# Kernel tuning notes

Measured on AMD Instinct MI355X. Metric: run time of the kernel, lower is better.

The kernel has to match this reference:

```python
import jax, jax.numpy as jnp
import numpy as np

N = 100000      # nodes
E = 1600000     # edges (avg degree 16)
F_IN = 512      # input node features
H = 8           # heads in conv1
D = 8           # per-head dim in conv1
C = 7           # classes
NEG_SLOPE = 0.2 # PyG GATConv default leaky_relu slope


def setup_inputs() -> dict:
    key = jax.random.key(0)
    ks = jax.random.split(key, 10)
    s = 0.05
    return {
        "x": jax.random.normal(ks[0], (N, F_IN), jnp.float32),
        "edge_index": jax.random.randint(ks[1], (2, E), 0, N, dtype=jnp.int64),
        "W1": jax.random.normal(ks[2], (F_IN, H * D), jnp.float32) * s,
        "a1_src": jax.random.normal(ks[3], (H, D), jnp.float32) * s,
        "a1_dst": jax.random.normal(ks[4], (H, D), jnp.float32) * s,
        "b1": jnp.zeros((H * D,), jnp.float32),
        "W2": jax.random.normal(ks[5], (H * D, C), jnp.float32) * s,
        "a2_src": jax.random.normal(ks[6], (1, C), jnp.float32) * s,
        "a2_dst": jax.random.normal(ks[7], (1, C), jnp.float32) * s,
        "b2": jnp.zeros((C,), jnp.float32),
    }


def _gat_conv(x, src, dst, W, a_src, a_dst, b, heads, dim, concat, n):
    # linear transform -> [N, H, D]
    h = (x @ W).reshape(n, heads, dim)
    # per-node attention halves: [N, H]
    al_src = jnp.einsum('nhd,hd->nh', h, a_src)
    al_dst = jnp.einsum('nhd,hd->nh', h, a_dst)
    # per-edge logits, leaky relu: [E', H]
    e = jax.nn.leaky_relu(al_src[src] + al_dst[dst], NEG_SLOPE)
    # segment softmax over incoming edges of each dst node
    m = jax.lax.stop_gradient(jax.ops.segment_max(e, dst, num_segments=n))
    p = jnp.exp(e - m[dst])
    z = jax.ops.segment_sum(p, dst, num_segments=n)
    alpha = p / z[dst]                                   # [E', H]
    # weighted scatter-add of source messages -> [N, H, D]
    out = jax.ops.segment_sum(h[src] * alpha[..., None], dst, num_segments=n)
    out = out.reshape(n, heads * dim) if concat else out.mean(axis=1)
    return out + b


def reference(x, edge_index, W1, a1_src, a1_dst, b1, W2, a2_src, a2_dst, b2):
    n = x.shape[0]
    # PyG GATConv default: add self loops
    loops = jnp.arange(n, dtype=edge_index.dtype)
    src = jnp.concatenate([edge_index[0], loops])
    dst = jnp.concatenate([edge_index[1], loops])
    h = _gat_conv(x, src, dst, W1, a1_src, a1_dst, b1, H, D, True, n)
    h = jax.nn.elu(h)
    out = _gat_conv(h, src, dst, W2, a2_src, a2_dst, b2, 1, C, False, n)
    return jax.nn.log_softmax(out, axis=1)
```

## Files before the change

### kernel.cpp

```cpp
#include <hip/hip_runtime.h>
#include <math.h>

#define N_NODES 100000
#define N_EDGES 1600000
#define F_IN 512
#define HD 64
#define CC 7
#define NKT (F_IN / 32)
#define BS 64
#define NBK ((N_NODES + BS - 1) / BS)
#define ECAP 2048
#define SCHUNK 4096
#define SBLK ((N_EDGES + SCHUNK - 1) / SCHUNK)

typedef __attribute__((ext_vector_type(8))) short short8;
typedef __attribute__((ext_vector_type(4))) float f32x4;

__device__ inline unsigned short f2bf(float f) {
    union { float f; unsigned u; } v; v.f = f;
    unsigned u = v.u;
    return (unsigned short)((u + 0x7fffu + ((u >> 16) & 1u)) >> 16);
}
__device__ inline float bf2f(unsigned short b) {
    union { unsigned u; float f; } v; v.u = ((unsigned)b) << 16;
    return v.f;
}

__global__ void zerob_kernel(int* __restrict__ bcur) {
    int i = blockIdx.x * 1024 + threadIdx.x;
    if (i < NBK) bcur[i] = 0;
}

__global__ void w1prep_kernel(const float* __restrict__ W1,
                              unsigned short* __restrict__ wf) {
    int t = blockIdx.x * 256 + threadIdx.x;
    if (t >= NKT * 4 * 64) return;
    int lane = t & 63;
    int ct = (t >> 6) & 3;
    int kt = t >> 8;
    int k0 = kt * 32 + (lane >> 4) * 8;
    int col = ct * 16 + (lane & 15);
    unsigned short* dst = wf + (size_t)t * 8;
    #pragma unroll
    for (int j = 0; j < 8; ++j) dst[j] = f2bf(W1[(k0 + j) * HD + col]);
}

__global__ __launch_bounds__(256) void gemm1att_kernel(const float* __restrict__ x,
                                                       const unsigned short* __restrict__ wf,
                                                       const float* __restrict__ a1s,
                                                       const float* __restrict__ a1d,
                                                       unsigned short* __restrict__ h1b,
                                                       float* __restrict__ als,
                                                       float* __restrict__ ald) {
    __shared__ float ls[64][65];
    const int wave = threadIdx.x >> 6;
    const int lane = threadIdx.x & 63;
    int arow = blockIdx.x * 64 + wave * 16 + (lane & 15);
    if (arow >= N_NODES) arow = N_NODES - 1;
    const float* xp = x + (size_t)arow * F_IN + (lane >> 4) * 8;
    const short8* wp = (const short8*)wf;

    f32x4 acc[4] = {};
    #pragma unroll 4
    for (int kt = 0; kt < NKT; ++kt) {
        f32x4 a0 = *(const f32x4*)(xp + kt * 32);
        f32x4 a1 = *(const f32x4*)(xp + kt * 32 + 4);
        union { short8 s; unsigned short u[8]; } af;
        af.u[0] = f2bf(a0.x); af.u[1] = f2bf(a0.y);
        af.u[2] = f2bf(a0.z); af.u[3] = f2bf(a0.w);
        af.u[4] = f2bf(a1.x); af.u[5] = f2bf(a1.y);
        af.u[6] = f2bf(a1.z); af.u[7] = f2bf(a1.w);
        #pragma unroll
        for (int ct = 0; ct < 4; ++ct) {
            short8 bf = wp[kt * 256 + ct * 64 + lane];
            acc[ct] = __builtin_amdgcn_mfma_f32_16x16x32_bf16(af.s, bf, acc[ct], 0, 0, 0);
        }
    }
    const int lrow_base = wave * 16 + (lane >> 4) * 4;
    const int ocol = lane & 15;
    #pragma unroll
    for (int ct = 0; ct < 4; ++ct) {
        #pragma unroll
        for (int r = 0; r < 4; ++r) {
            int lrow = lrow_base + r;
            int orow = blockIdx.x * 64 + lrow;
            ls[lrow][ct * 16 + ocol] = acc[ct][r];
            if (orow < N_NODES)
                h1b[(size_t)orow * HD + ct * 16 + ocol] = f2bf(acc[ct][r]);
        }
    }
    __syncthreads();
    #pragma unroll
    for (int task = threadIdx.x; task < 64 * 8; task += 256) {
        int r = task >> 3, h = task & 7;
        int node = blockIdx.x * 64 + r;
        if (node < N_NODES) {
            float s = 0.f, d = 0.f;
            #pragma unroll
            for (int k = 0; k < 8; ++k) {
                float v = ls[r][h * 8 + k];
                s += v * a1s[h * 8 + k];
                d += v * a1d[h * 8 + k];
            }
            als[node * 8 + h] = s;
            ald[node * 8 + h] = d;
        }
    }
}

__global__ __launch_bounds__(256) void binscatter_kernel(const int* __restrict__ ei,
                                                         int* __restrict__ bcur,
                                                         int2* __restrict__ pairs) {
    __shared__ int cnt[NBK];
    __shared__ int bas[NBK];
    const int e0 = blockIdx.x * SCHUNK;
    int e1 = e0 + SCHUNK; if (e1 > N_EDGES) e1 = N_EDGES;
    for (int b = threadIdx.x; b < NBK; b += 256) cnt[b] = 0;
    __syncthreads();
    for (int i = e0 + threadIdx.x; i < e1; i += 256)
        atomicAdd(&cnt[ei[N_EDGES + i] >> 6], 1);
    __syncthreads();
    for (int b = threadIdx.x; b < NBK; b += 256) {
        int c = cnt[b];
        bas[b] = c ? atomicAdd(&bcur[b], c) : 0;
        cnt[b] = 0;
    }
    __syncthreads();
    for (int i = e0 + threadIdx.x; i < e1; i += 256) {
        int s = ei[i];
        int t = ei[N_EDGES + i];
        int b = t >> 6;
        int pos = bas[b] + atomicAdd(&cnt[b], 1);
        if (pos < ECAP) pairs[(size_t)b * ECAP + pos] = make_int2(s, t);
    }
}

__global__ __launch_bounds__(256) void gather1_kernel(
        const int* __restrict__ bcur, const int2* __restrict__ pairs,
        const float* __restrict__ als, const float* __restrict__ ald,
        const unsigned short* __restrict__ h1b, const float* __restrict__ b1,
        const float* __restrict__ W2, const float* __restrict__ a2s,
        const float* __restrict__ a2d,
        unsigned short* __restrict__ g2b, float* __restrict__ al2s,
        float* __restrict__ al2d) {
    __shared__ int cnt[BS];
    __shared__ int start[BS];
    __shared__ int srcl[ECAP];
    const int tid = threadIdx.x;
    const int wave = tid >> 6, lane = tid & 63, h = lane >> 3;
    const int e8 = lane & 7, base8 = lane & 56;
    const int n0 = blockIdx.x * BS;
    const int2* bp = pairs + (size_t)blockIdx.x * ECAP;
    int ne = bcur[blockIdx.x]; if (ne > ECAP) ne = ECAP;
    if (tid < BS) cnt[tid] = 0;
    __syncthreads();
    for (int k = tid; k < ne; k += 256)
        atomicAdd(&cnt[bp[k].y & (BS - 1)], 1);
    __syncthreads();
    if (tid < 64) {
        int a = cnt[lane];
        int xx = a;
        #pragma unroll
        for (int o = 1; o < 64; o <<= 1) { int u = __shfl_up(xx, o, 64); if (lane >= o) xx += u; }
        start[lane] = xx - a;
        cnt[lane] = 0;
    }
    __syncthreads();
    for (int k = tid; k < ne; k += 256) {
        int2 pr = bp[k];
        int ln = pr.y & (BS - 1);
        int pos = start[ln] + atomicAdd(&cnt[ln], 1);
        srcl[pos] = pr.x;
    }
    __syncthreads();

    float w[CC];
    #pragma unroll
    for (int c = 0; c < CC; ++c) w[c] = W2[lane * CC + c];
    for (int n = wave * 16; n < wave * 16 + 16; ++n) {
        int node = n0 + n;
        if (node >= N_NODES) break;
        const float aldt = ald[node * 8 + h];
        float e = als[node * 8 + h] + aldt;
        e = (e >= 0.f) ? e : 0.2f * e;
        float p = __expf(e);
        float acc = p * bf2f(h1b[(size_t)node * HD + lane]);
        float z = p;
        int k = start[n];
        const int ke = k + cnt[n];
        for (; k + 8 <= ke; k += 8) {
            int s_own = srcl[k + e8];
            float ee = als[s_own * 8 + h] + aldt;
            ee = (ee >= 0.f) ? ee : 0.2f * ee;
            float pv = __expf(ee);
            #pragma unroll
            for (int q = 0; q < 8; ++q) {
                int se = srcl[k + q];
                float pe = __shfl(pv, base8 | q, 64);
                float ve = bf2f(h1b[(size_t)se * HD + lane]);
                z += pe;
                acc = fmaf(pe, ve, acc);
            }
        }
        if (k < ke) {
            const int m = ke - k;
            int idx = k + ((e8 < m) ? e8 : (m - 1));
            int s_own = srcl[idx];
            float ee = als[s_own * 8 + h] + aldt;
            ee = (ee >= 0.f) ? ee : 0.2f * ee;
            float pv = __expf(ee);
            for (int q = 0; q < m; ++q) {
                int se = srcl[k + q];
                float pe = __shfl(pv, base8 | q, 64);
                float ve = bf2f(h1b[(size_t)se * HD + lane]);
                z += pe;
                acc = fmaf(pe, ve, acc);
            }
        }
        float v = acc / z + b1[lane];
        v = (v > 0.f) ? v : (__expf(v) - 1.f);
        float g[CC];
        #pragma unroll
        for (int c = 0; c < CC; ++c) {
            float r = v * w[c];
            #pragma unroll
            for (int d = 1; d < 64; d <<= 1) r += __shfl_xor(r, d, 64);
            g[c] = r;
        }
        float s2 = 0.f, d2 = 0.f;
        #pragma unroll
        for (int c = 0; c < CC; ++c) { s2 += g[c] * a2s[c]; d2 += g[c] * a2d[c]; }
        if (lane < CC) g2b[(size_t)node * 8 + lane] = f2bf(g[lane]);
        if (lane == CC) g2b[(size_t)node * 8 + CC] = 0;
        if (lane == 8) al2s[node] = s2;
        if (lane == 9) al2d[node] = d2;
    }
}

__global__ __launch_bounds__(256) void gather2_kernel(
        const int* __restrict__ bcur, const int2* __restrict__ pairs,
        const float* __restrict__ al2s, const float* __restrict__ al2d,
        const unsigned short* __restrict__ g2b, const float* __restrict__ b2,
        float* __restrict__ out) {
    __shared__ int cnt[BS];
    __shared__ int start[BS];
    __shared__ int srcl[ECAP];
    const int tid = threadIdx.x;
    const int lane = tid & 63;
    const int grp = tid >> 3, c = tid & 7;
    const int base8 = lane & 56;
    const int n0 = blockIdx.x * BS;
    const int2* bp = pairs + (size_t)blockIdx.x * ECAP;
    int ne = bcur[blockIdx.x]; if (ne > ECAP) ne = ECAP;
    if (tid < BS) cnt[tid] = 0;
    __syncthreads();
    for (int k = tid; k < ne; k += 256)
        atomicAdd(&cnt[bp[k].y & (BS - 1)], 1);
    __syncthreads();
    if (tid < 64) {
        int a = cnt[lane];
        int xx = a;
        #pragma unroll
        for (int o = 1; o < 64; o <<= 1) { int u = __shfl_up(xx, o, 64); if (lane >= o) xx += u; }
        start[lane] = xx - a;
        cnt[lane] = 0;
    }
    __syncthreads();
    for (int k = tid; k < ne; k += 256) {
        int2 pr = bp[k];
        int ln = pr.y & (BS - 1);
        int pos = start[ln] + atomicAdd(&cnt[ln], 1);
        srcl[pos] = pr.x;
    }
    __syncthreads();

    for (int n = grp * 2; n < grp * 2 + 2; ++n) {
        int node = n0 + n;
        if (node >= N_NODES) break;
        const float adn = al2d[node];
        float e = al2s[node] + adn;
        e = (e >= 0.f) ? e : 0.2f * e;
        float p = __expf(e);
        float acc = p * bf2f(g2b[(size_t)node * 8 + c]);
        float z = p;
        int k = start[n];
        const int ke = k + cnt[n];
        for (; k + 8 <= ke; k += 8) {
            int s_own = srcl[k + c];
            float ee = al2s[s_own] + adn;
            ee = (ee >= 0.f) ? ee : 0.2f * ee;
            float pv = __expf(ee);
            #pragma unroll
            for (int q = 0; q < 8; ++q) {
                int se = srcl[k + q];
                float pe = __shfl(pv, base8 | q, 64);
                float ve = bf2f(g2b[(size_t)se * 8 + c]);
                z += pe;
                acc = fmaf(pe, ve, acc);
            }
        }
        if (k < ke) {
            const int m = ke - k;
            int idx = k + ((c < m) ? c : (m - 1));
            int s_own = srcl[idx];
            float ee = al2s[s_own] + adn;
            ee = (ee >= 0.f) ? ee : 0.2f * ee;
            float pv = __expf(ee);
            for (int q = 0; q < m; ++q) {
                int se = srcl[k + q];
                float pe = __shfl(pv, base8 | q, 64);
                float ve = bf2f(g2b[(size_t)se * 8 + c]);
                z += pe;
                acc = fmaf(pe, ve, acc);
            }
        }
        float o = (c < CC) ? (acc / z + b2[c]) : -1e30f;
        float m2 = o;
        #pragma unroll
        for (int d = 1; d < 8; d <<= 1) m2 = fmaxf(m2, __shfl_xor(m2, d, 8));
        float ex = (c < CC) ? __expf(o - m2) : 0.f;
        float sum = ex;
        #pragma unroll
        for (int d = 1; d < 8; d <<= 1) sum += __shfl_xor(sum, d, 8);
        float lse = m2 + __logf(sum);
        if (c < CC) out[(size_t)node * CC + c] = o - lse;
    }
}

extern "C" void kernel_launch(void* const* d_in, const int* in_sizes, int n_in,
                              void* d_out, int out_size, void* d_ws, size_t ws_size,
                              hipStream_t stream) {
    const float* x   = (const float*)d_in[0];
    const int*   ei  = (const int*)d_in[1];
    const float* W1  = (const float*)d_in[2];
    const float* a1s = (const float*)d_in[3];
    const float* a1d = (const float*)d_in[4];
    const float* b1  = (const float*)d_in[5];
    const float* W2  = (const float*)d_in[6];
    const float* a2s = (const float*)d_in[7];
    const float* a2d = (const float*)d_in[8];
    const float* b2  = (const float*)d_in[9];
    float* out = (float*)d_out;

    char* base = (char*)d_ws;
    size_t off = 0;
    auto alloc = [&](size_t bytes) { char* p = base + off; off = (off + bytes + 63) & ~(size_t)63; return p; };
    unsigned short* h1b = (unsigned short*)alloc((size_t)N_NODES * HD * 2);
    unsigned short* wf  = (unsigned short*)alloc((size_t)NKT * 4 * 64 * 8 * 2);
    float* als  = (float*)alloc((size_t)N_NODES * 8 * 4);
    float* ald  = (float*)alloc((size_t)N_NODES * 8 * 4);
    unsigned short* g2b = (unsigned short*)alloc((size_t)N_NODES * 8 * 2);
    float* al2s = (float*)alloc((size_t)N_NODES * 4);
    float* al2d = (float*)alloc((size_t)N_NODES * 4);
    int* bcur   = (int*)alloc((size_t)NBK * 4);
    int2* pairs = (int2*)alloc((size_t)NBK * ECAP * 8);

    zerob_kernel<<<(NBK + 1023) / 1024, 1024, 0, stream>>>(bcur);
    w1prep_kernel<<<(NKT * 4 * 64 + 255) / 256, 256, 0, stream>>>(W1, wf);
    binscatter_kernel<<<SBLK, 256, 0, stream>>>(ei, bcur, pairs);

    gemm1att_kernel<<<(N_NODES + 63) / 64, 256, 0, stream>>>(
        x, wf, a1s, a1d, h1b, als, ald);

    gather1_kernel<<<NBK, 256, 0, stream>>>(
        bcur, pairs, als, ald, h1b, b1, W2, a2s, a2d, g2b, al2s, al2d);
    gather2_kernel<<<NBK, 256, 0, stream>>>(
        bcur, pairs, al2s, al2d, g2b, b2, out);
}
```

Measured before the change: 239.9 us.

## Build per-node CSR once in a separate kernel and simplify gather kernels

Adds a sortcsr kernel that sorts each 64-node bin's edge pairs by destination once and writes a CSR source array plus per-node row pointers and counts. Both gather kernels then drop their duplicated shared-memory bucket sort. They map one wavefront (or one 8-lane group) per node over a much larger grid, and batch the eight neighbour feature loads ahead of the accumulation for more memory-level parallelism. The cost is one extra kernel launch and an extra global write and read of the CSR arrays.

```diff
diff --git a/kernel.cpp b/kernel.cpp
--- a/kernel.cpp
+++ b/kernel.cpp
@@ -135,196 +135,194 @@
     }
 }
 
+__global__ __launch_bounds__(256) void sortcsr_kernel(const int* __restrict__ bcur,
+                                                      const int2* __restrict__ pairs,
+                                                      int* __restrict__ csr_src,
+                                                      int* __restrict__ rowptr,
+                                                      int* __restrict__ rowcnt) {
+    __shared__ int cnt[BS];
+    __shared__ int start[BS];
+    __shared__ int srcl[ECAP];
+    const int tid = threadIdx.x;
+    const int lane = tid & 63;
+    const int n0 = blockIdx.x * BS;
+    const size_t bbase = (size_t)blockIdx.x * ECAP;
+    const int2* bp = pairs + bbase;
+    int ne = bcur[blockIdx.x]; if (ne > ECAP) ne = ECAP;
+    if (tid < BS) cnt[tid] = 0;
+    __syncthreads();
+    for (int k = tid; k < ne; k += 256)
+        atomicAdd(&cnt[bp[k].y & (BS - 1)], 1);
+    __syncthreads();
+    if (tid < 64) {
+        int a = cnt[lane];
+        int xx = a;
+        #pragma unroll
+        for (int o = 1; o < 64; o <<= 1) { int u = __shfl_up(xx, o, 64); if (lane >= o) xx += u; }
+        start[lane] = xx - a;
+        cnt[lane] = 0;
+    }
+    __syncthreads();
+    for (int k = tid; k < ne; k += 256) {
+        int2 pr = bp[k];
+        int ln = pr.y & (BS - 1);
+        int pos = start[ln] + atomicAdd(&cnt[ln], 1);
+        srcl[pos] = pr.x;
+    }
+    __syncthreads();
+    for (int k = tid; k < ne; k += 256) csr_src[bbase + k] = srcl[k];
+    if (tid < BS) {
+        int node = n0 + tid;
+        if (node < N_NODES) {
+            rowptr[node] = (int)bbase + start[tid];
+            rowcnt[node] = cnt[tid];
+        }
+    }
+}
+
 __global__ __launch_bounds__(256) void gather1_kernel(
-        const int* __restrict__ bcur, const int2* __restrict__ pairs,
+        const int* __restrict__ rowptr, const int* __restrict__ rowcnt,
+        const int* __restrict__ csr_src,
         const float* __restrict__ als, const float* __restrict__ ald,
         const unsigned short* __restrict__ h1b, const float* __restrict__ b1,
         const float* __restrict__ W2, const float* __restrict__ a2s,
         const float* __restrict__ a2d,
         unsigned short* __restrict__ g2b, float* __restrict__ al2s,
         float* __restrict__ al2d) {
-    __shared__ int cnt[BS];
-    __shared__ int start[BS];
-    __shared__ int srcl[ECAP];
-    const int tid = threadIdx.x;
-    const int wave = tid >> 6, lane = tid & 63, h = lane >> 3;
+    int node = (blockIdx.x * 256 + threadIdx.x) >> 6;
+    if (node >= N_NODES) return;
+    const int lane = threadIdx.x & 63;
+    const int h = lane >> 3;
     const int e8 = lane & 7, base8 = lane & 56;
-    const int n0 = blockIdx.x * BS;
-    const int2* bp = pairs + (size_t)blockIdx.x * ECAP;
-    int ne = bcur[blockIdx.x]; if (ne > ECAP) ne = ECAP;
-    if (tid < BS) cnt[tid] = 0;
-    __syncthreads();
-    for (int k = tid; k < ne; k += 256)
-        atomicAdd(&cnt[bp[k].y & (BS - 1)], 1);
-    __syncthreads();
-    if (tid < 64) {
-        int a = cnt[lane];
-        int xx = a;
-        #pragma unroll
-        for (int o = 1; o < 64; o <<= 1) { int u = __shfl_up(xx, o, 64); if (lane >= o) xx += u; }
-        start[lane] = xx - a;
-        cnt[lane] = 0;
-    }
-    __syncthreads();
-    for (int k = tid; k < ne; k += 256) {
-        int2 pr = bp[k];
-        int ln = pr.y & (BS - 1);
-        int pos = start[ln] + atomicAdd(&cnt[ln], 1);
-        srcl[pos] = pr.x;
-    }
-    __syncthreads();
-
+    const int rs = rowptr[node], ncnt = rowcnt[node];
+    const float aldt = ald[node * 8 + h];
+    float e = als[node * 8 + h] + aldt;
+    e = (e >= 0.f) ? e : 0.2f * e;
+    float p = __expf(e);
+    float acc = p * bf2f(h1b[(size_t)node * HD + lane]);
+    float z = p;
+    int k = 0;
+    for (; k + 8 <= ncnt; k += 8) {
+        int s_own = csr_src[rs + k + e8];
+        int se[8];
+        #pragma unroll
+        for (int q = 0; q < 8; ++q) se[q] = __shfl(s_own, base8 | q, 64);
+        float ve[8];
+        #pragma unroll
+        for (int q = 0; q < 8; ++q) ve[q] = bf2f(h1b[(size_t)se[q] * HD + lane]);
+        float ee = als[s_own * 8 + h] + aldt;
+        ee = (ee >= 0.f) ? ee : 0.2f * ee;
+        float pv = __expf(ee);
+        #pragma unroll
+        for (int q = 0; q < 8; ++q) {
+            float pe = __shfl(pv, base8 | q, 64);
+            z += pe;
+            acc = fmaf(pe, ve[q], acc);
+        }
+    }
+    if (k < ncnt) {
+        const int m = ncnt - k;
+        int idx = rs + k + ((e8 < m) ? e8 : (m - 1));
+        int s_own = csr_src[idx];
+        int se[8];
+        #pragma unroll
+        for (int q = 0; q < 8; ++q) se[q] = __shfl(s_own, base8 | q, 64);
+        float ee = als[s_own * 8 + h] + aldt;
+        ee = (ee >= 0.f) ? ee : 0.2f * ee;
+        float pv = __expf(ee);
+        for (int q = 0; q < m; ++q) {
+            float pe = __shfl(pv, base8 | q, 64);
+            float ve = bf2f(h1b[(size_t)se[q] * HD + lane]);
+            z += pe;
+            acc = fmaf(pe, ve, acc);
+        }
+    }
+    float v = acc / z + b1[lane];
+    v = (v > 0.f) ? v : (__expf(v) - 1.f);
     float w[CC];
     #pragma unroll
     for (int c = 0; c < CC; ++c) w[c] = W2[lane * CC + c];
-    for (int n = wave * 16; n < wave * 16 + 16; ++n) {
-        int node = n0 + n;
-        if (node >= N_NODES) break;
-        const float aldt = ald[node * 8 + h];
-        float e = als[node * 8 + h] + aldt;
-        e = (e >= 0.f) ? e : 0.2f * e;
-        float p = __expf(e);
-        float acc = p * bf2f(h1b[(size_t)node * HD + lane]);
-        float z = p;
-        int k = start[n];
-        const int ke = k + cnt[n];
-        for (; k + 8 <= ke; k += 8) {
-            int s_own = srcl[k + e8];
-            float ee = als[s_own * 8 + h] + aldt;
-            ee = (ee >= 0.f) ? ee : 0.2f * ee;
-            float pv = __expf(ee);
-            #pragma unroll
-            for (int q = 0; q < 8; ++q) {
-                int se = srcl[k + q];
-                float pe = __shfl(pv, base8 | q, 64);
-                float ve = bf2f(h1b[(size_t)se * HD + lane]);
-                z += pe;
-                acc = fmaf(pe, ve, acc);
-            }
-        }
-        if (k < ke) {
-            const int m = ke - k;
-            int idx = k + ((e8 < m) ? e8 : (m - 1));
-            int s_own = srcl[idx];
-            float ee = als[s_own * 8 + h] + aldt;
-            ee = (ee >= 0.f) ? ee : 0.2f * ee;
-            float pv = __expf(ee);
-            for (int q = 0; q < m; ++q) {
-                int se = srcl[k + q];
-                float pe = __shfl(pv, base8 | q, 64);
-                float ve = bf2f(h1b[(size_t)se * HD + lane]);
-                z += pe;
-                acc = fmaf(pe, ve, acc);
-            }
-        }
-        float v = acc / z + b1[lane];
-        v = (v > 0.f) ? v : (__expf(v) - 1.f);
-        float g[CC];
-        #pragma unroll
-        for (int c = 0; c < CC; ++c) {
-            float r = v * w[c];
-            #pragma unroll
-            for (int d = 1; d < 64; d <<= 1) r += __shfl_xor(r, d, 64);
-            g[c] = r;
-        }
-        float s2 = 0.f, d2 = 0.f;
-        #pragma unroll
-        for (int c = 0; c < CC; ++c) { s2 += g[c] * a2s[c]; d2 += g[c] * a2d[c]; }
-        if (lane < CC) g2b[(size_t)node * 8 + lane] = f2bf(g[lane]);
-        if (lane == CC) g2b[(size_t)node * 8 + CC] = 0;
-        if (lane == 8) al2s[node] = s2;
-        if (lane == 9) al2d[node] = d2;
-    }
+    float g[CC];
+    #pragma unroll
+    for (int c = 0; c < CC; ++c) {
+        float r = v * w[c];
+        #pragma unroll
+        for (int d = 1; d < 64; d <<= 1) r += __shfl_xor(r, d, 64);
+        g[c] = r;
+    }
+    float s2 = 0.f, d2 = 0.f;
+    #pragma unroll
+    for (int c = 0; c < CC; ++c) { s2 += g[c] * a2s[c]; d2 += g[c] * a2d[c]; }
+    if (lane < CC) g2b[(size_t)node * 8 + lane] = f2bf(g[lane]);
+    if (lane == CC) g2b[(size_t)node * 8 + CC] = 0;
+    if (lane == 8) al2s[node] = s2;
+    if (lane == 9) al2d[node] = d2;
 }
 
 __global__ __launch_bounds__(256) void gather2_kernel(
-        const int* __restrict__ bcur, const int2* __restrict__ pairs,
+        const int* __restrict__ rowptr, const int* __restrict__ rowcnt,
+        const int* __restrict__ csr_src,
         const float* __restrict__ al2s, const float* __restrict__ al2d,
         const unsigned short* __restrict__ g2b, const float* __restrict__ b2,
         float* __restrict__ out) {
-    __shared__ int cnt[BS];
-    __shared__ int start[BS];
-    __shared__ int srcl[ECAP];
-    const int tid = threadIdx.x;
-    const int lane = tid & 63;
-    const int grp = tid >> 3, c = tid & 7;
+    int gid = blockIdx.x * 256 + threadIdx.x;
+    int n = gid >> 3, c = gid & 7;
+    if (n >= N_NODES) return;
+    const int lane = threadIdx.x & 63;
     const int base8 = lane & 56;
-    const int n0 = blockIdx.x * BS;
-    const int2* bp = pairs + (size_t)blockIdx.x * ECAP;
-    int ne = bcur[blockIdx.x]; if (ne > ECAP) ne = ECAP;
-    if (tid < BS) cnt[tid] = 0;
-    __syncthreads();
-    for (int k = tid; k < ne; k += 256)
-        atomicAdd(&cnt[bp[k].y & (BS - 1)], 1);
-    __syncthreads();
-    if (tid < 64) {
-        int a = cnt[lane];
-        int xx = a;
-        #pragma unroll
-        for (int o = 1; o < 64; o <<= 1) { int u = __shfl_up(xx, o, 64); if (lane >= o) xx += u; }
-        start[lane] = xx - a;
-        cnt[lane] = 0;
-    }
-    __syncthreads();
-    for (int k = tid; k < ne; k += 256) {
-        int2 pr = bp[k];
-        int ln = pr.y & (BS - 1);
-        int pos = start[ln] + atomicAdd(&cnt[ln], 1);
-        srcl[pos] = pr.x;
-    }
-    __syncthreads();
-
-    for (int n = grp * 2; n < grp * 2 + 2; ++n) {
-        int node = n0 + n;
-        if (node >= N_NODES) break;
-        const float adn = al2d[node];
-        float e = al2s[node] + adn;
-        e = (e >= 0.f) ? e : 0.2f * e;
-        float p = __expf(e);
-        float acc = p * bf2f(g2b[(size_t)node * 8 + c]);
-        float z = p;
-        int k = start[n];
-        const int ke = k + cnt[n];
-        for (; k + 8 <= ke; k += 8) {
-            int s_own = srcl[k + c];
-            float ee = al2s[s_own] + adn;
-            ee = (ee >= 0.f) ? ee : 0.2f * ee;
-            float pv = __expf(ee);
-            #pragma unroll
-            for (int q = 0; q < 8; ++q) {
-                int se = srcl[k + q];
-                float pe = __shfl(pv, base8 | q, 64);
-                float ve = bf2f(g2b[(size_t)se * 8 + c]);
-                z += pe;
-                acc = fmaf(pe, ve, acc);
-            }
-        }
-        if (k < ke) {
-            const int m = ke - k;
-            int idx = k + ((c < m) ? c : (m - 1));
-            int s_own = srcl[idx];
-            float ee = al2s[s_own] + adn;
-            ee = (ee >= 0.f) ? ee : 0.2f * ee;
-            float pv = __expf(ee);
-            for (int q = 0; q < m; ++q) {
-                int se = srcl[k + q];
-                float pe = __shfl(pv, base8 | q, 64);
-                float ve = bf2f(g2b[(size_t)se * 8 + c]);
-                z += pe;
-                acc = fmaf(pe, ve, acc);
-            }
-        }
-        float o = (c < CC) ? (acc / z + b2[c]) : -1e30f;
-        float m2 = o;
-        #pragma unroll
-        for (int d = 1; d < 8; d <<= 1) m2 = fmaxf(m2, __shfl_xor(m2, d, 8));
-        float ex = (c < CC) ? __expf(o - m2) : 0.f;
-        float sum = ex;
-        #pragma unroll
-        for (int d = 1; d < 8; d <<= 1) sum += __shfl_xor(sum, d, 8);
-        float lse = m2 + __logf(sum);
-        if (c < CC) out[(size_t)node * CC + c] = o - lse;
-    }
+    const int rs = rowptr[n], ncnt = rowcnt[n];
+    const float adn = al2d[n];
+    float e = al2s[n] + adn;
+    e = (e >= 0.f) ? e : 0.2f * e;
+    float p = __expf(e);
+    float acc = p * bf2f(g2b[(size_t)n * 8 + c]);
+    float z = p;
+    int k = 0;
+    for (; k + 8 <= ncnt; k += 8) {
+        int s_own = csr_src[rs + k + c];
+        int se[8];
+        #pragma unroll
+        for (int q = 0; q < 8; ++q) se[q] = __shfl(s_own, base8 | q, 64);
+        float ve[8];
+        #pragma unroll
+        for (int q = 0; q < 8; ++q) ve[q] = bf2f(g2b[(size_t)se[q] * 8 + c]);
+        float ee = al2s[s_own] + adn;
+        ee = (ee >= 0.f) ? ee : 0.2f * ee;
+        float pv = __expf(ee);
+        #pragma unroll
+        for (int q = 0; q < 8; ++q) {
+            float pe = __shfl(pv, base8 | q, 64);
+            z += pe;
+            acc = fmaf(pe, ve[q], acc);
+        }
+    }
+    if (k < ncnt) {
+        const int m = ncnt - k;
+        int idx = rs + k + ((c < m) ? c : (m - 1));
+        int s_own = csr_src[idx];
+        int se[8];
+        #pragma unroll
+        for (int q = 0; q < 8; ++q) se[q] = __shfl(s_own, base8 | q, 64);
+        float ee = al2s[s_own] + adn;
+        ee = (ee >= 0.f) ? ee : 0.2f * ee;
+        float pv = __expf(ee);
+        for (int q = 0; q < m; ++q) {
+            float pe = __shfl(pv, base8 | q, 64);
+            float ve = bf2f(g2b[(size_t)se[q] * 8 + c]);
+            z += pe;
+            acc = fmaf(pe, ve, acc);
+        }
+    }
+    float o = (c < CC) ? (acc / z + b2[c]) : -1e30f;
+    float m2 = o;
+    #pragma unroll
+    for (int d = 1; d < 8; d <<= 1) m2 = fmaxf(m2, __shfl_xor(m2, d, 8));
+    float ex = (c < CC) ? __expf(o - m2) : 0.f;
+    float sum = ex;
+    #pragma unroll
+    for (int d = 1; d < 8; d <<= 1) sum += __shfl_xor(sum, d, 8);
+    float lse = m2 + __logf(sum);
+    if (c < CC) out[(size_t)n * CC + c] = o - lse;
 }
 
 extern "C" void kernel_launch(void* const* d_in, const int* in_sizes, int n_in,
@@ -353,17 +351,21 @@
     float* al2s = (float*)alloc((size_t)N_NODES * 4);
     float* al2d = (float*)alloc((size_t)N_NODES * 4);
     int* bcur   = (int*)alloc((size_t)NBK * 4);
+    int* rowptr = (int*)alloc((size_t)N_NODES * 4);
+    int* rowcnt = (int*)alloc((size_t)N_NODES * 4);
+    int* csr_src= (int*)alloc((size_t)NBK * ECAP * 4);
     int2* pairs = (int2*)alloc((size_t)NBK * ECAP * 8);
 
     zerob_kernel<<<(NBK + 1023) / 1024, 1024, 0, stream>>>(bcur);
     w1prep_kernel<<<(NKT * 4 * 64 + 255) / 256, 256, 0, stream>>>(W1, wf);
     binscatter_kernel<<<SBLK, 256, 0, stream>>>(ei, bcur, pairs);
+    sortcsr_kernel<<<NBK, 256, 0, stream>>>(bcur, pairs, csr_src, rowptr, rowcnt);
 
     gemm1att_kernel<<<(N_NODES + 63) / 64, 256, 0, stream>>>(
         x, wf, a1s, a1d, h1b, als, ald);
 
-    gather1_kernel<<<NBK, 256, 0, stream>>>(
-        bcur, pairs, als, ald, h1b, b1, W2, a2s, a2d, g2b, al2s, al2d);
-    gather2_kernel<<<NBK, 256, 0, stream>>>(
-        bcur, pairs, al2s, al2d, g2b, b2, out);
-}
+    gather1_kernel<<<(N_NODES * 64 + 255) / 256, 256, 0, stream>>>(
+        rowptr, rowcnt, csr_src, als, ald, h1b, b1, W2, a2s, a2d, g2b, al2s, al2d);
+    gather2_kernel<<<(N_NODES * 8 + 255) / 256, 256, 0, stream>>>(
+        rowptr, rowcnt, csr_src, al2s, al2d, g2b, b2, out);
+}
```

Result: faster. 223.5 us (-6.8%).
